# Kernel optimization log

Hardware: AMD Instinct MI355X
Metric: run time of the kernel (lower is better)

The kernel has to match this reference:

```python
import jax, jax.numpy as jnp
import numpy as np

EPS = 1e-5  # torch BatchNorm2d default


def _conv1x1(x, w):
    # x: [n, cin, h, w], w: [cout, cin] (1x1 conv == per-pixel matmul)
    return jnp.einsum('nchw,oc->nohw', x, w)


def _bn(x, gamma, beta, mean, var):
    # inference-mode BatchNorm2d over channel dim
    scale = gamma * jax.lax.rsqrt(var + EPS)
    shift = beta - mean * scale
    return x * scale[None, :, None, None] + shift[None, :, None, None]


def setup_inputs() -> dict:
    key = jax.random.key(0)
    ks = jax.random.split(key, 24)
    n, c, h, w = 16, 256, 64, 64
    width, planes = c // 2, c
    inp = {
        'x': jax.random.normal(ks[0], (n, c, h, w), jnp.float32),
        'w_theta': jax.random.normal(ks[1], (width, c), jnp.float32) * 0.05,
        'w_phi': jax.random.normal(ks[2], (width, c), jnp.float32) * 0.05,
        'w_g': jax.random.normal(ks[3], (width, c), jnp.float32) * 0.05,
        'w_zeta': jax.random.normal(ks[4], (planes, width), jnp.float32) * 0.05,
    }
    for i, (name, dim) in enumerate([('bn1', width), ('bn2', width), ('bn3', width), ('bn4', planes)]):
        k = 5 + 4 * i
        inp[f'{name}_gamma'] = jax.random.uniform(ks[k], (dim,), jnp.float32, 0.5, 1.5)
        inp[f'{name}_beta'] = jax.random.normal(ks[k + 1], (dim,), jnp.float32) * 0.1
        inp[f'{name}_mean'] = jax.random.normal(ks[k + 2], (dim,), jnp.float32) * 0.1
        inp[f'{name}_var'] = jax.random.uniform(ks[k + 3], (dim,), jnp.float32, 0.5, 1.5)
    return inp


def reference(x, w_theta, w_phi, w_g, w_zeta,
              bn1_gamma, bn1_beta, bn1_mean, bn1_var,
              bn2_gamma, bn2_beta, bn2_mean, bn2_var,
              bn3_gamma, bn3_beta, bn3_mean, bn3_var,
              bn4_gamma, bn4_beta, bn4_mean, bn4_var):
    n, c, h, w = x.shape
    theta = jax.nn.relu(_bn(_conv1x1(x, w_theta), bn1_gamma, bn1_beta, bn1_mean, bn1_var))
    phi = jax.nn.relu(_bn(_conv1x1(x, w_phi), bn2_gamma, bn2_beta, bn2_mean, bn2_var))
    g = jax.nn.relu(_bn(_conv1x1(x, w_g), bn3_gamma, bn3_beta, bn3_mean, bn3_var))

    width = theta.shape[1]
    hw = h * w
    theta = theta.reshape(n, width, hw)  # [n, C', S]
    phi = phi.reshape(n, width, hw)      # [n, C', S]
    g = g.reshape(n, width, hw)          # [n, C', S]

    # (theta^T @ phi) @ g^T == theta^T @ (phi @ g^T): no softmax, so associativity
    # lets us contract over pixels first -> O(S*C'^2) instead of O(S^2*C').
    kv = jnp.einsum('ncs,nds->ncd', phi, g)      # [n, C', C']
    out = jnp.einsum('ncs,ncd->nsd', theta, kv)  # [n, S, C']

    # faithful to torch: reshape (not transpose) [n, S, C'] -> [n, C', h, w]
    out = out.reshape(n, width, h, w)
    out = _bn(_conv1x1(out, w_zeta), bn4_gamma, bn4_beta, bn4_mean, bn4_var)
    return jax.nn.relu(out + x)
```

## Files before the change

### kernel.cpp

```cpp
#include <hip/hip_runtime.h>

#define BN_EPS 1e-5f

typedef unsigned short u16;
typedef __bf16 bf16x8 __attribute__((ext_vector_type(8)));
typedef float floatx4 __attribute__((ext_vector_type(4)));
typedef u16 u16x4 __attribute__((ext_vector_type(4)));
typedef u16 u16x8 __attribute__((ext_vector_type(8)));

__device__ __forceinline__ u16 f2bf(float f) {
    union { float f; unsigned int u; } v; v.f = f;
    unsigned int r = (v.u + 0x7fffu + ((v.u >> 16) & 1u)) >> 16;
    return (u16)r;
}

__device__ __forceinline__ unsigned int cvtpk(float lo, float hi) {
    unsigned int r;
    asm("v_cvt_pk_bf16_f32 %0, %1, %2" : "=v"(r) : "v"(lo), "v"(hi));
    return r;
}

__device__ __forceinline__ void gld16(const void* gsrc, void* ldst) {
    __builtin_amdgcn_global_load_lds(
        (const __attribute__((address_space(1))) unsigned int*)gsrc,
        (__attribute__((address_space(3))) unsigned int*)ldst, 16, 0, 0);
}

__device__ __forceinline__ int addsw(int seg, int s) {
    return (seg + (s & 7) + ((s >> 3) & 7)) & 7;
}

__global__ __launch_bounds__(256) void prep_kernel(
    const float* __restrict__ wt, const float* __restrict__ wp,
    const float* __restrict__ wg, const float* __restrict__ wz,
    const float* __restrict__ g1, const float* __restrict__ b1,
    const float* __restrict__ m1, const float* __restrict__ v1,
    const float* __restrict__ g2, const float* __restrict__ b2,
    const float* __restrict__ m2, const float* __restrict__ v2,
    const float* __restrict__ g3, const float* __restrict__ b3,
    const float* __restrict__ m3, const float* __restrict__ v3,
    const float* __restrict__ g4, const float* __restrict__ b4,
    const float* __restrict__ m4, const float* __restrict__ v4,
    u16* __restrict__ W1bf, float* __restrict__ shift1,
    u16* __restrict__ Wzbf, float* __restrict__ shift4)
{
    int id = blockIdx.x * 256 + threadIdx.x;
    if (id < 384 * 256) {
        int r = id >> 8, c = id & 255;
        int grp = r >> 7, ch = r & 127;
        const float* wsrc = grp == 0 ? wt : (grp == 1 ? wp : wg);
        const float* gg = grp == 0 ? g1 : (grp == 1 ? g2 : g3);
        const float* bb = grp == 0 ? b1 : (grp == 1 ? b2 : b3);
        const float* mm = grp == 0 ? m1 : (grp == 1 ? m2 : m3);
        const float* vv = grp == 0 ? v1 : (grp == 1 ? v2 : v3);
        float scale = gg[ch] * rsqrtf(vv[ch] + BN_EPS);
        W1bf[id] = f2bf(wsrc[ch * 256 + c] * scale);
        if (c == 0) shift1[r] = bb[ch] - mm[ch] * scale;
    }
    if (id < 256 * 128) {
        int o = id >> 7;
        float scale = g4[o] * rsqrtf(v4[o] + BN_EPS);
        Wzbf[id] = f2bf(wz[id] * scale);
        if ((id & 127) == 0) shift4[o] = b4[o] - m4[o] * scale;
    }
}

__global__ __launch_bounds__(512, 2) void k1_kernel(
    const float* __restrict__ x, const u16* __restrict__ W1,
    const float* __restrict__ shift1,
    u16* __restrict__ theta_sm, float* __restrict__ partials)
{
    const int sk = blockIdx.x, n = blockIdx.y;
    const int tid = threadIdx.x;
    const int w = tid >> 6, lane = tid & 63;
    const int quad = lane >> 4, l16 = lane & 15;

    __shared__ __align__(16) u16 pool[32768];
    u16* ldsA = pool;
    u16* ldsB = pool + 24576;

    floatx4 acc[3][8];
#pragma unroll
    for (int i = 0; i < 3; ++i)
#pragma unroll
        for (int j = 0; j < 8; ++j) acc[i][j] = floatx4{0.f, 0.f, 0.f, 0.f};

    const int cp = w * 4 + quad;
    const float* xb = x + ((size_t)n * 256 + 2 * cp) * 4096 + sk * 128;
    unsigned int* ldsBdw = (unsigned int*)ldsB;

    float4 xv[2][2];

    auto loadx = [&](int kc) {
#pragma unroll
        for (int ch = 0; ch < 2; ++ch)
#pragma unroll
            for (int hb = 0; hb < 2; ++hb)
                xv[ch][hb] = *((const float4*)(xb + (size_t)(kc * 64 + ch) * 4096) + hb * 16 + l16);
    };
    auto writeB = [&]() {
#pragma unroll
        for (int hb = 0; hb < 2; ++hb)
#pragma unroll
            for (int j = 0; j < 4; ++j) {
                int s = hb * 64 + l16 * 4 + j;
                ldsBdw[s * 32 + addsw(w, s) * 4 + quad] =
                    cvtpk(((const float*)&xv[0][hb])[j], ((const float*)&xv[1][hb])[j]);
            }
    };
    auto stageA = [&](int kc) {
#pragma unroll
        for (int i = 0; i < 6; ++i) {
            int op = w * 6 + i;
            int r = op * 8 + (lane >> 3);
            int lseg = (lane & 7) ^ (r & 7);
            gld16(W1 + (size_t)r * 256 + kc * 64 + lseg * 8, ldsA + op * 512);
        }
    };

    loadx(0);
    for (int kc = 0; kc < 4; ++kc) {
        writeB();
        if (kc < 3) loadx(kc + 1);
        stageA(kc);
        __syncthreads();
#pragma unroll
        for (int kk = 0; kk < 2; ++kk) {
            bf16x8 a[3];
#pragma unroll
            for (int mt = 0; mt < 3; ++mt) {
                int r = mt * 128 + w * 16 + l16;
                int phys = (kk * 4 + quad) ^ (r & 7);
                a[mt] = *(const bf16x8*)(ldsA + r * 64 + phys * 8);
            }
#pragma unroll
            for (int ni = 0; ni < 8; ++ni) {
                int s = ni * 16 + l16;
                int phys = addsw(kk * 4 + quad, s);
                bf16x8 b = *(const bf16x8*)(ldsB + s * 64 + phys * 8);
#pragma unroll
                for (int mt = 0; mt < 3; ++mt)
                    acc[mt][ni] = __builtin_amdgcn_mfma_f32_16x16x32_bf16(
                        a[mt], b, acc[mt][ni], 0, 0, 0);
            }
        }
        __syncthreads();
    }

    const int ocq = w * 16 + quad * 4;
    {
        float sh0 = shift1[ocq + 0], sh1 = shift1[ocq + 1];
        float sh2 = shift1[ocq + 2], sh3 = shift1[ocq + 3];
#pragma unroll
        for (int ni = 0; ni < 8; ++ni) {
            int s = sk * 128 + ni * 16 + l16;
            float v0 = acc[0][ni][0] + sh0, v1 = acc[0][ni][1] + sh1;
            float v2 = acc[0][ni][2] + sh2, v3 = acc[0][ni][3] + sh3;
            v0 = v0 > 0.f ? v0 : 0.f;
            v1 = v1 > 0.f ? v1 : 0.f;
            v2 = v2 > 0.f ? v2 : 0.f;
            v3 = v3 > 0.f ? v3 : 0.f;
            uint2 pk;
            pk.x = cvtpk(v0, v1);
            pk.y = cvtpk(v2, v3);
            *(uint2*)(theta_sm + (size_t)n * 524288 + (size_t)s * 128 + ocq) = pk;
        }
    }
#pragma unroll
    for (int mt = 1; mt < 3; ++mt)
#pragma unroll
        for (int r = 0; r < 4; ++r) {
            int ch = ocq + r;
            float sh = shift1[mt * 128 + ch];
#pragma unroll
            for (int ni = 0; ni < 8; ++ni) {
                int sl = ni * 16 + l16;
                int half = sl >> 6, s6 = sl & 63;
                int phys = (s6 >> 3) ^ (ch & 7);
                float val = acc[mt][ni][r] + sh;
                val = val > 0.f ? val : 0.f;
                pool[((mt - 1) * 2 + half) * 8192 + ch * 64 + phys * 8 + (s6 & 7)] = f2bf(val);
            }
        }
    __syncthreads();

    floatx4 kv[8];
#pragma unroll
    for (int i = 0; i < 8; ++i) kv[i] = floatx4{0.f, 0.f, 0.f, 0.f};
#pragma unroll
    for (int h = 0; h < 2; ++h)
#pragma unroll
        for (int kk = 0; kk < 2; ++kk) {
            int rd = w * 16 + l16;
            int physa = (kk * 4 + quad) ^ (rd & 7);
            bf16x8 a = *(const bf16x8*)(pool + (2 + h) * 8192 + rd * 64 + physa * 8);
#pragma unroll
            for (int ci = 0; ci < 8; ++ci) {
                int rc = ci * 16 + l16;
                int physb = (kk * 4 + quad) ^ (rc & 7);
                bf16x8 b = *(const bf16x8*)(pool + h * 8192 + rc * 64 + physb * 8);
                kv[ci] = __builtin_amdgcn_mfma_f32_16x16x32_bf16(a, b, kv[ci], 0, 0, 0);
            }
        }

    float* outp = partials + (size_t)(n * 32 + sk) * 16384;
#pragma unroll
    for (int r = 0; r < 4; ++r) {
        int d = w * 16 + quad * 4 + r;
#pragma unroll
        for (int ci = 0; ci < 8; ++ci)
            outp[d * 128 + ci * 16 + l16] = kv[ci][r];
    }
}

__global__ __launch_bounds__(256) void kv_reduce_kernel(
    const float* __restrict__ partials, u16* __restrict__ kvT)
{
    int n = blockIdx.y;
    int f4 = blockIdx.x * 256 + threadIdx.x;
    const float4* p4 = (const float4*)partials;
    float4 s = {0.f, 0.f, 0.f, 0.f};
#pragma unroll
    for (int kc = 0; kc < 32; ++kc) {
        float4 v = p4[(size_t)(n * 32 + kc) * 4096 + f4];
        s.x += v.x; s.y += v.y; s.z += v.z; s.w += v.w;
    }
    u16x4 o; o[0] = f2bf(s.x); o[1] = f2bf(s.y); o[2] = f2bf(s.z); o[3] = f2bf(s.w);
    *(u16x4*)(kvT + (size_t)n * 16384 + f4 * 4) = o;
}

__global__ __launch_bounds__(512, 2) void k34_kernel(
    const u16* __restrict__ theta_sm, const u16* __restrict__ kvT,
    const u16* __restrict__ Wz, const float* __restrict__ shift4,
    const float* __restrict__ x, float* __restrict__ out)
{
    const int st = blockIdx.x, n = blockIdx.y;
    const int tid = threadIdx.x;
    const int w = tid >> 6, lane = tid & 63;
    const int quad = lane >> 4, l16 = lane & 15;

    __shared__ __align__(16) u16 pool[32768];
    u16* Y = pool + 16384;

    const u16* tbase = theta_sm + (size_t)n * 524288 + (size_t)st * 128;
    const u16* kbase = kvT + (size_t)n * 16384;

    floatx4 acc3[8];
#pragma unroll
    for (int i = 0; i < 8; ++i) acc3[i] = floatx4{0.f, 0.f, 0.f, 0.f};

    auto stageTK = [&](u16* T, u16* K, int ch) {
#pragma unroll
        for (int i = 0; i < 2; ++i) {
            int op = w * 2 + i;
            int r = op * 8 + (lane >> 3);
            int lseg = (lane & 7) ^ (r & 7);
            gld16(tbase + (size_t)r * 4096 + ch * 64 + lseg * 8, T + op * 512);
            gld16(kbase + (size_t)r * 128 + ch * 64 + lseg * 8, K + op * 512);
        }
    };
    auto stageWz = [&](int ch) {
#pragma unroll
        for (int i = 0; i < 4; ++i) {
            int op = w * 4 + i;
            int r = op * 8 + (lane >> 3);
            int lseg = (lane & 7) ^ (r & 7);
            gld16(Wz + (size_t)r * 128 + ch * 64 + lseg * 8, pool + op * 512);
        }
    };
    auto comp3 = [&](const u16* T, const u16* K) {
#pragma unroll
        for (int kk = 0; kk < 2; ++kk) {
            int rc2 = w * 16 + l16;
            int physa = (kk * 4 + quad) ^ (rc2 & 7);
            bf16x8 a = *(const bf16x8*)(T + rc2 * 64 + physa * 8);
#pragma unroll
            for (int di = 0; di < 8; ++di) {
                int rd = di * 16 + l16;
                int physb = (kk * 4 + quad) ^ (rd & 7);
                bf16x8 b = *(const bf16x8*)(K + rd * 64 + physb * 8);
                acc3[di] = __builtin_amdgcn_mfma_f32_16x16x32_bf16(a, b, acc3[di], 0, 0, 0);
            }
        }
    };

    stageTK(pool, pool + 8192, 0);
    __syncthreads();
    stageTK(pool + 16384, pool + 24576, 1);
    comp3(pool, pool + 8192);
    __syncthreads();
    stageWz(0);
    comp3(pool + 16384, pool + 24576);
    __syncthreads();

#pragma unroll
    for (int di = 0; di < 8; ++di) {
        int j = di * 16 + l16;
#pragma unroll
        for (int r = 0; r < 4; ++r) {
            int c2 = w * 16 + quad * 4 + r;
            int half = c2 >> 6, c64 = c2 & 63;
            int phys = (c64 >> 3) ^ (j & 7);
            Y[half * 8192 + j * 64 + phys * 8 + (c64 & 7)] = f2bf(acc3[di][r]);
        }
    }
    __syncthreads();

    floatx4 acc4[2][8];
#pragma unroll
    for (int i = 0; i < 2; ++i)
#pragma unroll
        for (int j = 0; j < 8; ++j) acc4[i][j] = floatx4{0.f, 0.f, 0.f, 0.f};

    auto comp4 = [&](int ch) {
#pragma unroll
        for (int kk = 0; kk < 2; ++kk) {
            bf16x8 a[2];
#pragma unroll
            for (int mi = 0; mi < 2; ++mi) {
                int r = w * 32 + mi * 16 + l16;
                int phys = (kk * 4 + quad) ^ (r & 7);
                a[mi] = *(const bf16x8*)(pool + r * 64 + phys * 8);
            }
#pragma unroll
            for (int ni = 0; ni < 8; ++ni) {
                int s = ni * 16 + l16;
                int phys = (kk * 4 + quad) ^ (s & 7);
                bf16x8 b = *(const bf16x8*)(Y + ch * 8192 + s * 64 + phys * 8);
#pragma unroll
                for (int mi = 0; mi < 2; ++mi)
                    acc4[mi][ni] = __builtin_amdgcn_mfma_f32_16x16x32_bf16(
                        a[mi], b, acc4[mi][ni], 0, 0, 0);
            }
        }
    };

    comp4(0);
    __syncthreads();
    stageWz(1);
    __syncthreads();
    comp4(1);

#pragma unroll
    for (int mi = 0; mi < 2; ++mi)
#pragma unroll
        for (int r = 0; r < 4; ++r) {
            int o = w * 32 + mi * 16 + quad * 4 + r;
            float sh = shift4[o];
#pragma unroll
            for (int ni = 0; ni < 8; ++ni) {
                int s2 = st * 128 + ni * 16 + l16;
                size_t idx = ((size_t)n * 256 + o) * 4096 + s2;
                float val = acc4[mi][ni][r] + sh + x[idx];
                out[idx] = val > 0.f ? val : 0.f;
            }
        }
}

extern "C" void kernel_launch(void* const* d_in, const int* in_sizes, int n_in,
                              void* d_out, int out_size, void* d_ws, size_t ws_size,
                              hipStream_t stream)
{
    const float* x  = (const float*)d_in[0];
    const float* wt = (const float*)d_in[1];
    const float* wp = (const float*)d_in[2];
    const float* wg = (const float*)d_in[3];
    const float* wz = (const float*)d_in[4];
    const float* bn[16];
    for (int i = 0; i < 16; ++i) bn[i] = (const float*)d_in[5 + i];

    char* ws = (char*)d_ws;
    u16*   W1bf     = (u16*)  (ws + 0);
    float* shift1   = (float*)(ws + 196608);
    u16*   Wzbf     = (u16*)  (ws + 198144);
    float* shift4   = (float*)(ws + 263680);
    u16*   theta_sm = (u16*)  (ws + 264704);
    float* partials = (float*)(ws + 17041920);
    u16*   kvT      = (u16*)  (ws + 50596352);
    float* out = (float*)d_out;

    prep_kernel<<<384, 256, 0, stream>>>(
        wt, wp, wg, wz,
        bn[0], bn[1], bn[2], bn[3],
        bn[4], bn[5], bn[6], bn[7],
        bn[8], bn[9], bn[10], bn[11],
        bn[12], bn[13], bn[14], bn[15],
        W1bf, shift1, Wzbf, shift4);

    k1_kernel<<<dim3(32, 16), 512, 0, stream>>>(x, W1bf, shift1, theta_sm, partials);
    kv_reduce_kernel<<<dim3(16, 16), 256, 0, stream>>>(partials, kvT);
    k34_kernel<<<dim3(32, 16), 512, 0, stream>>>(theta_sm, kvT, Wzbf, shift4, x, out);
}
```

Measured before the change: 198.7 us.

## Store kv partials in bf16 and double-buffer x register prefetch in k1

```diff
diff --git a/kernel.cpp b/kernel.cpp
--- a/kernel.cpp
+++ b/kernel.cpp
@@ -12,6 +12,11 @@
     union { float f; unsigned int u; } v; v.f = f;
     unsigned int r = (v.u + 0x7fffu + ((v.u >> 16) & 1u)) >> 16;
     return (u16)r;
+}
+
+__device__ __forceinline__ float bf2f(u16 b) {
+    union { unsigned int u; float f; } v; v.u = ((unsigned int)b) << 16;
+    return v.f;
 }
 
 __device__ __forceinline__ unsigned int cvtpk(float lo, float hi) {
@@ -68,7 +73,7 @@
 __global__ __launch_bounds__(512, 2) void k1_kernel(
     const float* __restrict__ x, const u16* __restrict__ W1,
     const float* __restrict__ shift1,
-    u16* __restrict__ theta_sm, float* __restrict__ partials)
+    u16* __restrict__ theta_sm, u16* __restrict__ partials)
 {
     const int sk = blockIdx.x, n = blockIdx.y;
     const int tid = threadIdx.x;
@@ -89,16 +94,16 @@
     const float* xb = x + ((size_t)n * 256 + 2 * cp) * 4096 + sk * 128;
     unsigned int* ldsBdw = (unsigned int*)ldsB;
 
-    float4 xv[2][2];
-
-    auto loadx = [&](int kc) {
+    float4 xva[2][2], xvb[2][2];
+
+    auto loadx = [&](float4 (&xv)[2][2], int kc) {
 #pragma unroll
         for (int ch = 0; ch < 2; ++ch)
 #pragma unroll
             for (int hb = 0; hb < 2; ++hb)
                 xv[ch][hb] = *((const float4*)(xb + (size_t)(kc * 64 + ch) * 4096) + hb * 16 + l16);
     };
-    auto writeB = [&]() {
+    auto writeB = [&](const float4 (&xv)[2][2]) {
 #pragma unroll
         for (int hb = 0; hb < 2; ++hb)
 #pragma unroll
@@ -117,13 +122,7 @@
             gld16(W1 + (size_t)r * 256 + kc * 64 + lseg * 8, ldsA + op * 512);
         }
     };
-
-    loadx(0);
-    for (int kc = 0; kc < 4; ++kc) {
-        writeB();
-        if (kc < 3) loadx(kc + 1);
-        stageA(kc);
-        __syncthreads();
+    auto compute = [&]() {
 #pragma unroll
         for (int kk = 0; kk < 2; ++kk) {
             bf16x8 a[3];
@@ -144,8 +143,18 @@
                         a[mt], b, acc[mt][ni], 0, 0, 0);
             }
         }
-        __syncthreads();
-    }
+    };
+
+    loadx(xva, 0);
+    loadx(xvb, 1);
+    writeB(xva); loadx(xva, 2); stageA(0);
+    __syncthreads(); compute(); __syncthreads();
+    writeB(xvb); loadx(xvb, 3); stageA(1);
+    __syncthreads(); compute(); __syncthreads();
+    writeB(xva); stageA(2);
+    __syncthreads(); compute(); __syncthreads();
+    writeB(xvb); stageA(3);
+    __syncthreads(); compute(); __syncthreads();
 
     const int ocq = w * 16 + quad * 4;
     {
@@ -203,29 +212,28 @@
             }
         }
 
-    float* outp = partials + (size_t)(n * 32 + sk) * 16384;
+    u16* outp = partials + (size_t)(n * 32 + sk) * 16384;
 #pragma unroll
     for (int r = 0; r < 4; ++r) {
         int d = w * 16 + quad * 4 + r;
 #pragma unroll
         for (int ci = 0; ci < 8; ++ci)
-            outp[d * 128 + ci * 16 + l16] = kv[ci][r];
+            outp[d * 128 + ci * 16 + l16] = f2bf(kv[ci][r]);
     }
 }
 
 __global__ __launch_bounds__(256) void kv_reduce_kernel(
-    const float* __restrict__ partials, u16* __restrict__ kvT)
+    const u16* __restrict__ partials, u16* __restrict__ kvT)
 {
     int n = blockIdx.y;
     int f4 = blockIdx.x * 256 + threadIdx.x;
-    const float4* p4 = (const float4*)partials;
-    float4 s = {0.f, 0.f, 0.f, 0.f};
+    float s0 = 0.f, s1 = 0.f, s2 = 0.f, s3 = 0.f;
 #pragma unroll
     for (int kc = 0; kc < 32; ++kc) {
-        float4 v = p4[(size_t)(n * 32 + kc) * 4096 + f4];
-        s.x += v.x; s.y += v.y; s.z += v.z; s.w += v.w;
-    }
-    u16x4 o; o[0] = f2bf(s.x); o[1] = f2bf(s.y); o[2] = f2bf(s.z); o[3] = f2bf(s.w);
+        u16x4 v = *(const u16x4*)(partials + (size_t)(n * 32 + kc) * 16384 + f4 * 4);
+        s0 += bf2f(v[0]); s1 += bf2f(v[1]); s2 += bf2f(v[2]); s3 += bf2f(v[3]);
+    }
+    u16x4 o; o[0] = f2bf(s0); o[1] = f2bf(s1); o[2] = f2bf(s2); o[3] = f2bf(s3);
     *(u16x4*)(kvT + (size_t)n * 16384 + f4 * 4) = o;
 }
 
@@ -375,8 +383,8 @@
     u16*   Wzbf     = (u16*)  (ws + 198144);
     float* shift4   = (float*)(ws + 263680);
     u16*   theta_sm = (u16*)  (ws + 264704);
-    float* partials = (float*)(ws + 17041920);
-    u16*   kvT      = (u16*)  (ws + 50596352);
+    u16*   partials = (u16*)  (ws + 17041920);
+    u16*   kvT      = (u16*)  (ws + 33819136);
     float* out = (float*)d_out;
 
     prep_kernel<<<384, 256, 0, stream>>>(
```

New measurement: 193.9 us. 1.02x faster.
